# Kernel optimization log

Hardware: AMD Instinct MI355X
Metric: run time of the kernel (lower is better)

Reference implementation:

```python
import jax, jax.numpy as jnp
import numpy as np

HIDDEN = 1024
HEADS = 16
HEAD_DIM = HIDDEN // HEADS
SCALE = HEAD_DIM ** (-0.5)


def setup_inputs() -> dict:
    key = jax.random.key(0)
    ks = jax.random.split(key, 5)
    B, N, C = 8, 1024, HIDDEN
    x = jax.random.normal(ks[0], (B, N, C), dtype=jnp.float32)
    # torch nn.Linear params: weight [out, in], bias [out]
    w_in = jax.random.normal(ks[1], (3 * C, C), dtype=jnp.float32) * (C ** -0.5)
    b_in = jax.random.normal(ks[2], (3 * C,), dtype=jnp.float32) * 0.02
    w_out = jax.random.normal(ks[3], (C, C), dtype=jnp.float32) * (C ** -0.5)
    b_out = jax.random.normal(ks[4], (C,), dtype=jnp.float32) * 0.02
    return {"x": x, "w_in": w_in, "b_in": b_in, "w_out": w_out, "b_out": b_out}


def reference(x, w_in, b_in, w_out, b_out):
    B, N, C = x.shape
    H, D = HEADS, HEAD_DIM
    # in_proj: [B,N,3C] -> (3,B,H,N,D)
    qkv = x @ w_in.T + b_in
    qkv = qkv.reshape(B, N, 3, H, D).transpose(2, 0, 3, 1, 4)
    q, k, v = qkv[0], qkv[1], qkv[2]
    # attention scores scaled after QK^T (same math as scaling q)
    attn = jnp.einsum("bhnd,bhmd->bhnm", q, k) * SCALE
    attn = jax.nn.softmax(attn, axis=-1)
    out = jnp.einsum("bhnm,bhmd->bhnd", attn, v)  # [B,H,N,D]
    out = out.transpose(0, 2, 1, 3).reshape(B, N, C)
    return out @ w_out.T + b_out
```

## Files before the change

kernel.cpp:

```cpp
#include <hip/hip_runtime.h>


typedef __attribute__((ext_vector_type(8))) __bf16 bf16x8;
typedef __attribute__((ext_vector_type(4))) __bf16 bf16x4;
typedef __attribute__((ext_vector_type(4))) float f32x4;
typedef __attribute__((ext_vector_type(4))) short short4v;

__device__ __forceinline__ f32x4 mfma16(bf16x8 a, bf16x8 b, f32x4 c) {
  return __builtin_amdgcn_mfma_f32_16x16x32_bf16(a, b, c, 0, 0, 0);
}

#if __has_builtin(__builtin_amdgcn_mfma_f32_16x16x16bf16_1k)
__device__ __forceinline__ f32x4 mfma_pv(bf16x4 a, bf16x4 b, f32x4 c) {
  short4v as = __builtin_bit_cast(short4v, a);
  short4v bs = __builtin_bit_cast(short4v, b);
  return __builtin_amdgcn_mfma_f32_16x16x16bf16_1k(as, bs, c, 0, 0, 0);
}
#else
__device__ __forceinline__ f32x4 mfma_pv(bf16x4 a, bf16x4 b, f32x4 c) {
  __bf16 z = (__bf16)0.f;
  bf16x8 a8 = {a[0], a[1], a[2], a[3], z, z, z, z};
  bf16x8 b8 = {b[0], b[1], b[2], b[3], z, z, z, z};
  return mfma16(a8, b8, c);
}
#endif

__device__ __forceinline__ float fexp2(float x) {
#if __has_builtin(__builtin_amdgcn_exp2f)
  return __builtin_amdgcn_exp2f(x);
#else
  return exp2f(x);
#endif
}

typedef __attribute__((address_space(1))) const unsigned int gu32;
typedef __attribute__((address_space(3))) unsigned int lu32;

__device__ __forceinline__ void async16(const void* g, void* l) {
  __builtin_amdgcn_global_load_lds((gu32*)g, (lu32*)l, 16, 0, 0);
}

__global__ __launch_bounds__(256) void cvt_all(const float* __restrict__ x,
                                               __bf16* __restrict__ xb,
                                               const float* __restrict__ wi,
                                               __bf16* __restrict__ wib,
                                               const float* __restrict__ wo,
                                               __bf16* __restrict__ wob) {
  int blk = blockIdx.x;
  const float* in;
  __bf16* out;
  int base;
  if (blk < 4096)      { in = x;  out = xb;  base = 0; }
  else if (blk < 5632) { in = wi; out = wib; base = 4096; }
  else                 { in = wo; out = wob; base = 5632; }
  int i = ((blk - base) * 256 + threadIdx.x) * 8;
  float4 a = *(const float4*)(in + i);
  float4 b = *(const float4*)(in + i + 4);
  bf16x8 o;
  o[0] = (__bf16)a.x; o[1] = (__bf16)a.y; o[2] = (__bf16)a.z; o[3] = (__bf16)a.w;
  o[4] = (__bf16)b.x; o[5] = (__bf16)b.y; o[6] = (__bf16)b.z; o[7] = (__bf16)b.w;
  *(bf16x8*)(out + i) = o;
}

template <int NB, bool WRITE_VT, typename OutT>
__global__ __launch_bounds__(256) void gemm_nt(const __bf16* __restrict__ A,
                                               const __bf16* __restrict__ Bm,
                                               const float* __restrict__ bias,
                                               OutT* __restrict__ C, int K, int ldc,
                                               __bf16* __restrict__ vt) {
  __shared__ __bf16 As[128 * 64];
  __shared__ __bf16 Bs[NB * 32 * 64];
  const int t = threadIdx.x;
  const int wv = t >> 6, lane = t & 63;
  const int q16 = lane & 15, quad = lane >> 4;
  const int wm = wv >> 1, wn = wv & 1;
  const long m0 = (long)blockIdx.x * 128;
  const long n0 = (long)blockIdx.y * (NB * 32);

  f32x4 zero = {0.f, 0.f, 0.f, 0.f};
  f32x4 acc[4][NB];
#pragma unroll
  for (int i = 0; i < 4; ++i)
#pragma unroll
    for (int j = 0; j < NB; ++j) acc[i][j] = zero;

  char* AsB = (char*)As;
  char* BsB = (char*)Bs;
  const int sr = t >> 3;
  const int gc = (t & 7) ^ (sr & 7);

  for (int kt = 0; kt < K; kt += 64) {
    __syncthreads();
#pragma unroll
    for (int i = 0; i < 4; ++i)
      async16(A + (m0 + i * 32 + sr) * K + kt + gc * 8, AsB + i * 4096 + wv * 1024);
#pragma unroll
    for (int i = 0; i < NB; ++i)
      async16(Bm + (n0 + i * 32 + sr) * K + kt + gc * 8, BsB + i * 4096 + wv * 1024);
    __syncthreads();

#pragma unroll
    for (int kk = 0; kk < 2; ++kk) {
      bf16x8 af[4], bf[NB];
#pragma unroll
      for (int i = 0; i < 4; ++i) {
        int ra = wm * 64 + i * 16 + q16;
        af[i] = *(const bf16x8*)(AsB + ra * 128 + (((kk * 4 + quad) ^ (ra & 7)) * 16));
      }
#pragma unroll
      for (int j = 0; j < NB; ++j) {
        int rb = wn * (NB * 16) + j * 16 + q16;
        bf[j] = *(const bf16x8*)(BsB + rb * 128 + (((kk * 4 + quad) ^ (rb & 7)) * 16));
      }
#pragma unroll
      for (int i = 0; i < 4; ++i)
#pragma unroll
        for (int j = 0; j < NB; ++j) acc[i][j] = mfma16(af[i], bf[j], acc[i][j]);
    }
  }

  if (WRITE_VT && n0 >= 2048) {
    const int b = (int)(m0 >> 10);
    const int nbase = (int)(m0 - (long)b * 1024) + wm * 64;
#pragma unroll
    for (int j = 0; j < NB; ++j) {
      int col = (int)n0 + wn * (NB * 16) + j * 16 + q16;
      int cc = col - 2048;
      int h = cc >> 6, d = cc & 63;
      float bs = bias[col];
      __bf16* vrow = vt + (((long)(b * 16 + h)) << 16) + (long)d * 1024;
#pragma unroll
      for (int i = 0; i < 4; ++i) {
        int n = nbase + i * 16 + quad * 4;
        bf16x4 o;
#pragma unroll
        for (int r = 0; r < 4; ++r) o[r] = (__bf16)(acc[i][j][r] + bs);
        *(bf16x4*)(vrow + n) = o;
      }
    }
  } else {
#pragma unroll
    for (int j = 0; j < NB; ++j) {
      long col = n0 + wn * (NB * 16) + j * 16 + q16;
      float bs = bias[col];
#pragma unroll
      for (int i = 0; i < 4; ++i) {
        long rowb = m0 + wm * 64 + i * 16 + quad * 4;
#pragma unroll
        for (int r = 0; r < 4; ++r) {
          float v = acc[i][j][r] + bs;
          C[(rowb + r) * (long)ldc + col] = (OutT)v;
        }
      }
    }
  }
}

template <typename OutT>
__global__ __launch_bounds__(256) void gemm_nt64(const __bf16* __restrict__ A,
                                                 const __bf16* __restrict__ Bm,
                                                 const float* __restrict__ bias,
                                                 OutT* __restrict__ C, int K, int ldc) {
  __shared__ __bf16 As[64 * 64];
  __shared__ __bf16 Bs[128 * 64];
  const int t = threadIdx.x;
  const int wv = t >> 6, lane = t & 63;
  const int q16 = lane & 15, quad = lane >> 4;
  const int wm = wv >> 1, wn = wv & 1;
  const long m0 = (long)blockIdx.x * 64;
  const long n0 = (long)blockIdx.y * 128;

  f32x4 zero = {0.f, 0.f, 0.f, 0.f};
  f32x4 acc[2][4];
#pragma unroll
  for (int i = 0; i < 2; ++i)
#pragma unroll
    for (int j = 0; j < 4; ++j) acc[i][j] = zero;

  char* AsB = (char*)As;
  char* BsB = (char*)Bs;
  const int sr = t >> 3;
  const int gc = (t & 7) ^ (sr & 7);

  for (int kt = 0; kt < K; kt += 64) {
    __syncthreads();
#pragma unroll
    for (int i = 0; i < 2; ++i)
      async16(A + (m0 + i * 32 + sr) * K + kt + gc * 8, AsB + i * 4096 + wv * 1024);
#pragma unroll
    for (int i = 0; i < 4; ++i)
      async16(Bm + (n0 + i * 32 + sr) * K + kt + gc * 8, BsB + i * 4096 + wv * 1024);
    __syncthreads();

#pragma unroll
    for (int kk = 0; kk < 2; ++kk) {
      bf16x8 af[2], bf[4];
#pragma unroll
      for (int i = 0; i < 2; ++i) {
        int ra = wm * 32 + i * 16 + q16;
        af[i] = *(const bf16x8*)(AsB + ra * 128 + (((kk * 4 + quad) ^ (ra & 7)) * 16));
      }
#pragma unroll
      for (int j = 0; j < 4; ++j) {
        int rb = wn * 64 + j * 16 + q16;
        bf[j] = *(const bf16x8*)(BsB + rb * 128 + (((kk * 4 + quad) ^ (rb & 7)) * 16));
      }
#pragma unroll
      for (int i = 0; i < 2; ++i)
#pragma unroll
        for (int j = 0; j < 4; ++j) acc[i][j] = mfma16(af[i], bf[j], acc[i][j]);
    }
  }

#pragma unroll
  for (int j = 0; j < 4; ++j) {
    long col = n0 + wn * 64 + j * 16 + q16;
    float bs = bias[col];
#pragma unroll
    for (int i = 0; i < 2; ++i) {
      long rowb = m0 + wm * 32 + i * 16 + quad * 4;
#pragma unroll
      for (int r = 0; r < 4; ++r) {
        float v = acc[i][j][r] + bs;
        C[(rowb + r) * (long)ldc + col] = (OutT)v;
      }
    }
  }
}

__global__ __launch_bounds__(256) void attn_kernel(const __bf16* __restrict__ qkv,
                                                   const __bf16* __restrict__ vt,
                                                   __bf16* __restrict__ ao) {
  __shared__ __bf16 Ks[64 * 64];
  __shared__ __bf16 Vt[64 * 64];
  const int t = threadIdx.x;
  const int wv = t >> 6, lane = t & 63;
  const int q16 = lane & 15, quad = lane >> 4;
  const int bh = blockIdx.x;
  const int b = bh >> 4, h = bh & 15;
  const int q0 = blockIdx.y * 64;
  const long rowbase = (long)b * 1024;

  bf16x8 qf0, qf1;
  {
    long qrow = rowbase + q0 + wv * 16 + q16;
    const __bf16* qp = qkv + qrow * 3072 + h * 64 + quad * 8;
    qf0 = *(const bf16x8*)qp;
    qf1 = *(const bf16x8*)(qp + 32);
#pragma unroll
    for (int j = 0; j < 8; ++j) {
      qf0[j] = (__bf16)((float)qf0[j] * 0.18033688f);
      qf1[j] = (__bf16)((float)qf1[j] * 0.18033688f);
    }
  }

  f32x4 zero = {0.f, 0.f, 0.f, 0.f};
  f32x4 oacc[4];
#pragma unroll
  for (int dt = 0; dt < 4; ++dt) oacc[dt] = zero;
  float lcol = 0.f;

  char* KsB = (char*)Ks;
  char* VtB = (char*)Vt;
  const int sr = t >> 3;
  const int sgc = (t & 7) ^ (sr & 7);
  const int sw = q16 & 7;

  for (int kv0 = 0; kv0 < 1024; kv0 += 64) {
    __syncthreads();
    const __bf16* kg = qkv + (rowbase + kv0 + sr) * 3072 + 1024 + h * 64 + sgc * 8;
    async16(kg, KsB + wv * 1024);
    async16(kg + (long)32 * 3072, KsB + 4096 + wv * 1024);
    const __bf16* vg = vt + (long)bh * 65536 + (long)sr * 1024 + kv0 + sgc * 8;
    async16(vg, VtB + wv * 1024);
    async16(vg + (long)32 * 1024, VtB + 4096 + wv * 1024);
    __syncthreads();

    f32x4 sacc[4];
#pragma unroll
    for (int nt = 0; nt < 4; ++nt) sacc[nt] = zero;
#pragma unroll
    for (int nt = 0; nt < 4; ++nt) {
      int kvr = nt * 16 + q16;
      bf16x8 kf0 = *(const bf16x8*)(KsB + kvr * 128 + ((quad ^ sw) * 16));
      bf16x8 kf1 = *(const bf16x8*)(KsB + kvr * 128 + (((4 + quad) ^ sw) * 16));
      sacc[nt] = mfma16(kf0, qf0, sacc[nt]);
      sacc[nt] = mfma16(kf1, qf1, sacc[nt]);
    }

    bf16x4 pf[4];
#pragma unroll
    for (int nt = 0; nt < 4; ++nt)
#pragma unroll
      for (int r = 0; r < 4; ++r) {
        float p = fexp2(sacc[nt][r]);
        lcol += p;
        pf[nt][r] = (__bf16)p;
      }

#pragma unroll
    for (int nt = 0; nt < 4; ++nt) {
      int c = ((nt * 2 + (quad >> 1)) ^ sw) * 16 + (quad & 1) * 8;
#pragma unroll
      for (int dt = 0; dt < 4; ++dt) {
        bf16x4 vf = *(const bf16x4*)(VtB + (dt * 16 + q16) * 128 + c);
        oacc[dt] = mfma_pv(pf[nt], vf, oacc[dt]);
      }
    }
  }

  lcol += __shfl_xor(lcol, 16);
  lcol += __shfl_xor(lcol, 32);
  float inv = 1.0f / lcol;
#pragma unroll
  for (int r = 0; r < 4; ++r) {
    float ir = __shfl(inv, quad * 4 + r);
    long orow = rowbase + q0 + wv * 16 + quad * 4 + r;
#pragma unroll
    for (int dt = 0; dt < 4; ++dt)
      ao[orow * 1024 + h * 64 + dt * 16 + q16] = (__bf16)(oacc[dt][r] * ir);
  }
}

extern "C" void kernel_launch(void* const* d_in, const int* in_sizes, int n_in,
                              void* d_out, int out_size, void* d_ws, size_t ws_size,
                              hipStream_t stream) {
  const float* x     = (const float*)d_in[0];
  const float* w_in  = (const float*)d_in[1];
  const float* b_in  = (const float*)d_in[2];
  const float* w_out = (const float*)d_in[3];
  const float* b_out = (const float*)d_in[4];
  float* out = (float*)d_out;

  char* ws = (char*)d_ws;
  __bf16* xb   = (__bf16*)(ws);
  __bf16* wib  = (__bf16*)(ws + 16777216);
  __bf16* wob  = (__bf16*)(ws + 23068672);
  __bf16* qkvb = (__bf16*)(ws + 25165824);
  __bf16* aob  = (__bf16*)(ws + 75497472);
  __bf16* vtg  = (__bf16*)d_out;

  cvt_all<<<6144, 256, 0, stream>>>(x, xb, w_in, wib, w_out, wob);
  gemm_nt<4, true, __bf16><<<dim3(64, 24), 256, 0, stream>>>(
      xb, wib, b_in, qkvb, 1024, 3072, vtg);
  attn_kernel<<<dim3(128, 16), 256, 0, stream>>>(qkvb, vtg, aob);
  gemm_nt64<float><<<dim3(128, 8), 256, 0, stream>>>(
      aob, wob, b_out, out, 1024, 1024);
}
```

Baseline: 247.3 us.

## Load GEMM and attention K operands directly from global memory, bypassing LDS

The output-projection GEMM drops its LDS staging and __syncthreads pairs; each wave now reads its A and B MFMA fragments straight from global memory in 32-wide K steps. The attention kernel likewise stops staging K tiles in shared memory and loads K fragments directly from the qkv buffer, keeping LDS only for V^T. This removes LDS traffic and barrier cost but gives up cross-wave reuse, so each wave fetches redundant data and relies on the cache. It also adds strided, lower-coalescing global loads.

After: 379.3 us. +53.4%, slower.

```diff
diff --git a/kernel.cpp b/kernel.cpp
--- a/kernel.cpp
+++ b/kernel.cpp
@@ -157,12 +157,10 @@
 }
 
 template <typename OutT>
-__global__ __launch_bounds__(256) void gemm_nt64(const __bf16* __restrict__ A,
-                                                 const __bf16* __restrict__ Bm,
-                                                 const float* __restrict__ bias,
-                                                 OutT* __restrict__ C, int K, int ldc) {
-  __shared__ __bf16 As[64 * 64];
-  __shared__ __bf16 Bs[128 * 64];
+__global__ __launch_bounds__(256) void gemm2_direct(const __bf16* __restrict__ A,
+                                                    const __bf16* __restrict__ Bm,
+                                                    const float* __restrict__ bias,
+                                                    OutT* __restrict__ C, int K, int ldc) {
   const int t = threadIdx.x;
   const int wv = t >> 6, lane = t & 63;
   const int q16 = lane & 15, quad = lane >> 4;
@@ -177,39 +175,22 @@
 #pragma unroll
     for (int j = 0; j < 4; ++j) acc[i][j] = zero;
 
-  char* AsB = (char*)As;
-  char* BsB = (char*)Bs;
-  const int sr = t >> 3;
-  const int gc = (t & 7) ^ (sr & 7);
-
-  for (int kt = 0; kt < K; kt += 64) {
-    __syncthreads();
+  const __bf16* ap0 = A + (m0 + wm * 32 + q16) * (long)K + quad * 8;
+  const __bf16* ap1 = ap0 + 16 * (long)K;
+  const __bf16* bp0 = Bm + (n0 + wn * 64 + q16) * (long)K + quad * 8;
+
+#pragma unroll 2
+  for (int kt = 0; kt < K; kt += 32) {
+    bf16x8 af[2], bf[4];
+    af[0] = *(const bf16x8*)(ap0 + kt);
+    af[1] = *(const bf16x8*)(ap1 + kt);
+#pragma unroll
+    for (int j = 0; j < 4; ++j)
+      bf[j] = *(const bf16x8*)(bp0 + j * 16 * (long)K + kt);
 #pragma unroll
     for (int i = 0; i < 2; ++i)
-      async16(A + (m0 + i * 32 + sr) * K + kt + gc * 8, AsB + i * 4096 + wv * 1024);
-#pragma unroll
-    for (int i = 0; i < 4; ++i)
-      async16(Bm + (n0 + i * 32 + sr) * K + kt + gc * 8, BsB + i * 4096 + wv * 1024);
-    __syncthreads();
-
-#pragma unroll
-    for (int kk = 0; kk < 2; ++kk) {
-      bf16x8 af[2], bf[4];
-#pragma unroll
-      for (int i = 0; i < 2; ++i) {
-        int ra = wm * 32 + i * 16 + q16;
-        af[i] = *(const bf16x8*)(AsB + ra * 128 + (((kk * 4 + quad) ^ (ra & 7)) * 16));
-      }
-#pragma unroll
-      for (int j = 0; j < 4; ++j) {
-        int rb = wn * 64 + j * 16 + q16;
-        bf[j] = *(const bf16x8*)(BsB + rb * 128 + (((kk * 4 + quad) ^ (rb & 7)) * 16));
-      }
-#pragma unroll
-      for (int i = 0; i < 2; ++i)
-#pragma unroll
-        for (int j = 0; j < 4; ++j) acc[i][j] = mfma16(af[i], bf[j], acc[i][j]);
-    }
+#pragma unroll
+      for (int j = 0; j < 4; ++j) acc[i][j] = mfma16(af[i], bf[j], acc[i][j]);
   }
 
 #pragma unroll
@@ -231,7 +212,6 @@
 __global__ __launch_bounds__(256) void attn_kernel(const __bf16* __restrict__ qkv,
                                                    const __bf16* __restrict__ vt,
                                                    __bf16* __restrict__ ao) {
-  __shared__ __bf16 Ks[64 * 64];
   __shared__ __bf16 Vt[64 * 64];
   const int t = threadIdx.x;
   const int wv = t >> 6, lane = t & 63;
@@ -260,17 +240,15 @@
   for (int dt = 0; dt < 4; ++dt) oacc[dt] = zero;
   float lcol = 0.f;
 
-  char* KsB = (char*)Ks;
   char* VtB = (char*)Vt;
   const int sr = t >> 3;
   const int sgc = (t & 7) ^ (sr & 7);
   const int sw = q16 & 7;
 
+  const __bf16* kb = qkv + (rowbase + q16) * 3072 + 1024 + h * 64 + quad * 8;
+
   for (int kv0 = 0; kv0 < 1024; kv0 += 64) {
     __syncthreads();
-    const __bf16* kg = qkv + (rowbase + kv0 + sr) * 3072 + 1024 + h * 64 + sgc * 8;
-    async16(kg, KsB + wv * 1024);
-    async16(kg + (long)32 * 3072, KsB + 4096 + wv * 1024);
     const __bf16* vg = vt + (long)bh * 65536 + (long)sr * 1024 + kv0 + sgc * 8;
     async16(vg, VtB + wv * 1024);
     async16(vg + (long)32 * 1024, VtB + 4096 + wv * 1024);
@@ -281,9 +259,9 @@
     for (int nt = 0; nt < 4; ++nt) sacc[nt] = zero;
 #pragma unroll
     for (int nt = 0; nt < 4; ++nt) {
-      int kvr = nt * 16 + q16;
-      bf16x8 kf0 = *(const bf16x8*)(KsB + kvr * 128 + ((quad ^ sw) * 16));
-      bf16x8 kf1 = *(const bf16x8*)(KsB + kvr * 128 + (((4 + quad) ^ sw) * 16));
+      const __bf16* kp = kb + (long)(kv0 + nt * 16) * 3072;
+      bf16x8 kf0 = *(const bf16x8*)kp;
+      bf16x8 kf1 = *(const bf16x8*)(kp + 32);
       sacc[nt] = mfma16(kf0, qf0, sacc[nt]);
       sacc[nt] = mfma16(kf1, qf1, sacc[nt]);
     }
@@ -344,6 +322,6 @@
   gemm_nt<4, true, __bf16><<<dim3(64, 24), 256, 0, stream>>>(
       xb, wib, b_in, qkvb, 1024, 3072, vtg);
   attn_kernel<<<dim3(128, 16), 256, 0, stream>>>(qkvb, vtg, aob);
-  gemm_nt64<float><<<dim3(128, 8), 256, 0, stream>>>(
+  gemm2_direct<float><<<dim3(128, 8), 256, 0, stream>>>(
       aob, wob, b_out, out, 1024, 1024);
 }
```
